# Performance work log

Hardware: AMD Instinct MI355X
Metric: run time of the kernel (lower is better)

The kernel has to match this reference:

```python
import jax, jax.numpy as jnp
import numpy as np

N, P, D = 8, 4096, 3


def _chamfer_one_direction(x, y, x_lengths, y_lengths):
    # x: (N,P1,D), y: (N,P2,D); squared-L2 k=1 NN of each x point in y (norm=2 in knn_points)
    P1 = x.shape[1]
    P2 = y.shape[1]
    x2 = jnp.sum(x * x, axis=-1)  # (N,P1)
    y2 = jnp.sum(y * y, axis=-1)  # (N,P2)
    d2 = x2[:, :, None] + y2[:, None, :] - 2.0 * jnp.einsum('npd,nqd->npq', x, y)  # (N,P1,P2)
    # mask padded y points out of the NN search
    y_mask = jnp.arange(P2)[None, :] >= y_lengths[:, None]  # (N,P2) True = padded
    d2 = jnp.where(y_mask[:, None, :], jnp.inf, d2)
    cham = jnp.min(d2, axis=2)  # (N,P1) dist to nearest valid y
    # zero out padded x points
    x_mask = jnp.arange(P1)[None, :] >= x_lengths[:, None]  # (N,P1)
    cham = jnp.where(x_mask, 0.0, cham)
    # point_reduction='mean'
    per_cloud = jnp.sum(cham, axis=1) / jnp.maximum(x_lengths, 1).astype(x.dtype)  # (N,)
    # batch_reduction='mean' (no weights -> divide by N)
    return jnp.sum(per_cloud) / x.shape[0]


def setup_inputs() -> dict:
    key = jax.random.key(0)
    k1, k2, k3, k4 = jax.random.split(key, 4)
    x = jax.random.normal(k1, (N, P, D), dtype=jnp.float32)
    y = jax.random.normal(k2, (N, P, D), dtype=jnp.float32)
    x_lengths = jax.random.randint(k3, (N,), P // 2, P + 1)
    y_lengths = jax.random.randint(k4, (N,), P // 2, P + 1)
    return {"x": x, "y": y, "x_lengths": x_lengths, "y_lengths": y_lengths}


def reference(x, y, x_lengths, y_lengths):
    cham_x = _chamfer_one_direction(x, y, x_lengths, y_lengths)
    cham_y = _chamfer_one_direction(y, x, y_lengths, x_lengths)
    return cham_x + cham_y
```

## Files before the change

kernel.cpp:

```cpp
#include <hip/hip_runtime.h>
#include <hip/hip_bf16.h>
#include <math.h>

constexpr int NB  = 8;
constexpr int PP  = 4096;

constexpr int TPB = 256;
constexpr int XPT = 8;
constexpr int XCH = TPB * XPT;
constexpr int NXC = PP / XCH;
constexpr int NYC = 32;
constexpr int JH  = 2;
constexpr int JCH = 64;
constexpr int NCH = NYC * JH;
constexpr int GRIDA = 2 * NB * NXC * NYC * JH;

constexpr int NSEG = 16;
constexpr int SEGP = PP / NSEG;
constexpr int NPART = 2 * NB * NSEG;

__global__ __launch_bounds__(TPB, 4) void nn_partial(
    const float* __restrict__ x, const float* __restrict__ y,
    const int* __restrict__ xlen, const int* __restrict__ ylen,
    float* __restrict__ ws)
{
    __shared__ float4 sy[JCH];

    const int bid = (int)blockIdx.x;
    const int jh  = bid & (JH - 1);
    const int yc  = (bid >> 1) & (NYC - 1);
    const int xc  = (bid >> 6) & (NXC - 1);
    const int n   = (bid >> 7) & (NB - 1);
    const int dir = bid >> 10;

    const float* __restrict__ xs = dir ? y : x;
    const float* __restrict__ ys = dir ? x : y;
    const int yl = (dir ? xlen : ylen)[n];
    const int ql = (dir ? ylen : xlen)[n];

    const float* __restrict__ yb = ys + (size_t)n * PP * 3;
    if ((int)threadIdx.x < JCH) {
        const int p   = (int)threadIdx.x;
        const int idx = yc + NYC * (jh * JCH + p);
        float y0 = yb[idx * 3 + 0];
        float y1 = yb[idx * 3 + 1];
        float y2 = yb[idx * 3 + 2];
        sy[p] = make_float4(-2.f * y0, -2.f * y1, -2.f * y2,
                            fmaf(y0, y0, fmaf(y1, y1, y2 * y2)));
    }

    const int wave  = (int)threadIdx.x >> 6;
    const int lane  = (int)threadIdx.x & 63;
    const int wbase = xc * XCH + wave * (XPT * 64);

    float px0[XPT], px1[XPT], px2[XPT], a[XPT], emin[XPT];
    const float* __restrict__ xb = xs + (size_t)n * PP * 3;
#pragma unroll
    for (int k = 0; k < XPT; ++k) {
        const int xi = wbase + k * 64 + lane;
        px0[k] = xb[xi * 3 + 0];
        px1[k] = xb[xi * 3 + 1];
        px2[k] = xb[xi * 3 + 2];
        a[k]   = fmaf(px0[k], px0[k], fmaf(px1[k], px1[k], px2[k] * px2[k]));
        emin[k] = INFINITY;
    }
    __syncthreads();

    int jslice = (yl - yc + NYC - 1) >> 5;
    int jcnt = jslice - jh * JCH;
    if (jcnt > JCH) jcnt = JCH;

    if (ql > wbase && jcnt > 0) {
        const int j2 = jcnt & ~1;
#pragma unroll 2
        for (int j = 0; j < j2; j += 2) {
            const float4 u = sy[j];
            const float4 v = sy[j + 1];
#pragma unroll
            for (int k = 0; k < XPT; ++k) {
                float e1 = fmaf(px0[k], u.x, fmaf(px1[k], u.y, fmaf(px2[k], u.z, u.w)));
                float e2 = fmaf(px0[k], v.x, fmaf(px1[k], v.y, fmaf(px2[k], v.z, v.w)));
                emin[k] = fminf(emin[k], fminf(e1, e2));
            }
        }
        if (jcnt & 1) {
            const float4 u = sy[jcnt - 1];
#pragma unroll
            for (int k = 0; k < XPT; ++k) {
                float e1 = fmaf(px0[k], u.x, fmaf(px1[k], u.y, fmaf(px2[k], u.z, u.w)));
                emin[k] = fminf(emin[k], e1);
            }
        }
    }

    float* __restrict__ w = ws + ((size_t)(dir * NB + n) * NCH + (yc * JH + jh)) * PP;
#pragma unroll
    for (int k = 0; k < XPT; ++k) {
        w[wbase + k * 64 + lane] = a[k] + emin[k];
    }
}

__global__ __launch_bounds__(256) void reduce_cloud(
    const float* __restrict__ ws,
    const int* __restrict__ xlen, const int* __restrict__ ylen,
    float* __restrict__ partial)
{
    const int b   = blockIdx.x;
    const int seg = b & (NSEG - 1);
    const int c   = b >> 4;
    const int dir = c >> 3;
    const int n   = c & (NB - 1);
    const int xl  = (dir ? ylen : xlen)[n];

    const float* __restrict__ w = ws + (size_t)c * NCH * PP;
    const int i = seg * SEGP + (int)threadIdx.x;

    float m = w[i];
#pragma unroll
    for (int ch = 1; ch < NCH; ++ch) m = fminf(m, w[(size_t)ch * PP + i]);
    float sum = (i < xl) ? m : 0.f;

#pragma unroll
    for (int off = 32; off > 0; off >>= 1) sum += __shfl_xor(sum, off);
    __shared__ float ls[4];
    const int lane = (int)threadIdx.x & 63;
    const int wv   = (int)threadIdx.x >> 6;
    if (lane == 0) ls[wv] = sum;
    __syncthreads();
    if (threadIdx.x == 0) {
        float tot = ls[0] + ls[1] + ls[2] + ls[3];
        int d = xl > 1 ? xl : 1;
        partial[b] = tot / (float)d / (float)NB;
    }
}

__global__ __launch_bounds__(256) void final_sum(
    const float* __restrict__ partial, float* __restrict__ out)
{
    float v = partial[threadIdx.x];
#pragma unroll
    for (int off = 32; off > 0; off >>= 1) v += __shfl_xor(v, off);
    __shared__ float ls[4];
    const int lane = (int)threadIdx.x & 63;
    const int wv   = (int)threadIdx.x >> 6;
    if (lane == 0) ls[wv] = v;
    __syncthreads();
    if (threadIdx.x == 0) out[0] = ls[0] + ls[1] + ls[2] + ls[3];
}

__global__ __launch_bounds__(TPB) void chamfer_atomic(
    const float* __restrict__ x, const float* __restrict__ y,
    const int* __restrict__ xlen, const int* __restrict__ ylen,
    float* __restrict__ out)
{
    __shared__ float4 sy[JCH];

    int bid = blockIdx.x;
    const int xc  = bid & (NXC - 1);
    const int n   = (bid >> 1) & (NB - 1);
    const int dir = bid >> 4;

    const float* __restrict__ xs = dir ? y : x;
    const float* __restrict__ ys = dir ? x : y;
    const int yl = (dir ? xlen : ylen)[n];
    const int xl = (dir ? ylen : xlen)[n];

    float px0[XPT], px1[XPT], px2[XPT], a[XPT], emin[XPT];
    const int wave  = (int)threadIdx.x >> 6;
    const int lane  = (int)threadIdx.x & 63;
    const int wbase = xc * XCH + wave * (XPT * 64);
    const float* __restrict__ xb = xs + (size_t)n * PP * 3;
#pragma unroll
    for (int k = 0; k < XPT; ++k) {
        const int xi = wbase + k * 64 + lane;
        px0[k] = xb[xi * 3 + 0];
        px1[k] = xb[xi * 3 + 1];
        px2[k] = xb[xi * 3 + 2];
        a[k]   = fmaf(px0[k], px0[k], fmaf(px1[k], px1[k], px2[k] * px2[k]));
        emin[k] = INFINITY;
    }

    const float* __restrict__ yb = ys + (size_t)n * PP * 3;
    for (int half = 0; half < NYC * JH; ++half) {
        const int yc = half >> 1, jh = half & 1;
        __syncthreads();
        if ((int)threadIdx.x < JCH) {
            const int p   = (int)threadIdx.x;
            const int idx = yc + NYC * (jh * JCH + p);
            float y0 = yb[idx * 3 + 0];
            float y1 = yb[idx * 3 + 1];
            float y2 = yb[idx * 3 + 2];
            sy[p] = make_float4(-2.f * y0, -2.f * y1, -2.f * y2,
                                fmaf(y0, y0, fmaf(y1, y1, y2 * y2)));
        }
        __syncthreads();
        int jslice = (yl - yc + NYC - 1) >> 5;
        int jcnt = jslice - jh * JCH;
        if (jcnt > JCH) jcnt = JCH;
        for (int j = 0; j < jcnt; ++j) {
            const float4 u = sy[j];
#pragma unroll
            for (int k = 0; k < XPT; ++k) {
                float e = fmaf(px0[k], u.x, fmaf(px1[k], u.y, fmaf(px2[k], u.z, u.w)));
                emin[k] = fminf(emin[k], e);
            }
        }
    }

    float sum = 0.f;
#pragma unroll
    for (int k = 0; k < XPT; ++k) {
        const int xi = wbase + k * 64 + lane;
        if (xi < xl) sum += a[k] + emin[k];
    }
#pragma unroll
    for (int off = 32; off > 0; off >>= 1) sum += __shfl_xor(sum, off);
    __shared__ float ls[4];
    if (lane == 0) ls[wave] = sum;
    __syncthreads();
    if (threadIdx.x == 0) {
        float tot = ls[0] + ls[1] + ls[2] + ls[3];
        int d = xl > 1 ? xl : 1;
        atomicAdd(out, tot / (float)d / (float)NB);
    }
}

extern "C" void kernel_launch(void* const* d_in, const int* in_sizes, int n_in,
                              void* d_out, int out_size, void* d_ws, size_t ws_size,
                              hipStream_t stream) {
    const float* x  = (const float*)d_in[0];
    const float* y  = (const float*)d_in[1];
    const int* xl   = (const int*)d_in[2];
    const int* yl   = (const int*)d_in[3];
    float* out      = (float*)d_out;

    const size_t ws_floats = (size_t)2 * NB * NCH * PP;
    const size_t ws_need   = (ws_floats + NPART) * sizeof(float);

    if (ws_size >= ws_need) {
        float* ws      = (float*)d_ws;
        float* partial = ws + ws_floats;
        nn_partial<<<GRIDA, TPB, 0, stream>>>(x, y, xl, yl, ws);
        reduce_cloud<<<NPART, 256, 0, stream>>>(ws, xl, yl, partial);
        final_sum<<<1, 256, 0, stream>>>(partial, out);
    } else {
        hipMemsetAsync(d_out, 0, sizeof(float), stream);
        const int gridF = 2 * NB * NXC;
        chamfer_atomic<<<gridF, TPB, 0, stream>>>(x, y, xl, yl, out);
    }
}
```

Measured before the change: 33.26 us.

## Replace per-chunk partial-min workspace with atomicMin into compact ordered-key table

Instead of each block writing its partial nearest-neighbour minima to a large per-y-chunk workspace that a second kernel min-reduces, blocks now atomicMin an order-preserving uint encoding of the distance into one entry per query point. The table is initialised with a memset, and a single-block kernel decodes, masks and averages all clouds, replacing the two reduction kernels. Each block now covers 128 y points with 4 x points per thread. This removes the multi-megabyte workspace write and read-back, but adds global atomics and a memset, and makes the final reduction serial on one workgroup.

```diff
diff --git a/kernel.cpp b/kernel.cpp
--- a/kernel.cpp
+++ b/kernel.cpp
@@ -4,32 +4,35 @@
 
 constexpr int NB  = 8;
 constexpr int PP  = 4096;
+constexpr int NC  = 2 * NB;
 
 constexpr int TPB = 256;
-constexpr int XPT = 8;
+constexpr int XPT = 4;
 constexpr int XCH = TPB * XPT;
 constexpr int NXC = PP / XCH;
 constexpr int NYC = 32;
-constexpr int JH  = 2;
-constexpr int JCH = 64;
-constexpr int NCH = NYC * JH;
-constexpr int GRIDA = 2 * NB * NXC * NYC * JH;
-
-constexpr int NSEG = 16;
-constexpr int SEGP = PP / NSEG;
-constexpr int NPART = 2 * NB * NSEG;
+constexpr int YCH = PP / NYC;
+constexpr int GRIDA = 2 * NB * NXC * NYC;
+
+__device__ inline unsigned int fkey(float f) {
+    unsigned int b = __float_as_uint(f);
+    return (b & 0x80000000u) ? ~b : (b | 0x80000000u);
+}
+__device__ inline float fdecode(unsigned int k) {
+    unsigned int b = (k & 0x80000000u) ? (k & 0x7FFFFFFFu) : ~k;
+    return __uint_as_float(b);
+}
 
 __global__ __launch_bounds__(TPB, 4) void nn_partial(
     const float* __restrict__ x, const float* __restrict__ y,
     const int* __restrict__ xlen, const int* __restrict__ ylen,
-    float* __restrict__ ws)
+    unsigned int* __restrict__ tab)
 {
-    __shared__ float4 sy[JCH];
+    __shared__ float4 sy[YCH];
 
     const int bid = (int)blockIdx.x;
-    const int jh  = bid & (JH - 1);
-    const int yc  = (bid >> 1) & (NYC - 1);
-    const int xc  = (bid >> 6) & (NXC - 1);
+    const int yc  = bid & (NYC - 1);
+    const int xc  = (bid >> 5) & (NXC - 1);
     const int n   = (bid >> 7) & (NB - 1);
     const int dir = bid >> 10;
 
@@ -39,9 +42,9 @@
     const int ql = (dir ? ylen : xlen)[n];
 
     const float* __restrict__ yb = ys + (size_t)n * PP * 3;
-    if ((int)threadIdx.x < JCH) {
+    if ((int)threadIdx.x < YCH) {
         const int p   = (int)threadIdx.x;
-        const int idx = yc + NYC * (jh * JCH + p);
+        const int idx = yc + NYC * p;
         float y0 = yb[idx * 3 + 0];
         float y1 = yb[idx * 3 + 1];
         float y2 = yb[idx * 3 + 2];
@@ -66,12 +69,11 @@
     }
     __syncthreads();
 
-    int jslice = (yl - yc + NYC - 1) >> 5;
-    int jcnt = jslice - jh * JCH;
-    if (jcnt > JCH) jcnt = JCH;
-
-    if (ql > wbase && jcnt > 0) {
-        const int j2 = jcnt & ~1;
+    int jend = (yl - yc + NYC - 1) >> 5;
+    if (jend > YCH) jend = YCH;
+
+    if (ql > wbase) {
+        const int j2 = jend & ~1;
 #pragma unroll 2
         for (int j = 0; j < j2; j += 2) {
             const float4 u = sy[j];
@@ -83,69 +85,74 @@
                 emin[k] = fminf(emin[k], fminf(e1, e2));
             }
         }
-        if (jcnt & 1) {
-            const float4 u = sy[jcnt - 1];
+        if (jend & 1) {
+            const float4 u = sy[jend - 1];
 #pragma unroll
             for (int k = 0; k < XPT; ++k) {
                 float e1 = fmaf(px0[k], u.x, fmaf(px1[k], u.y, fmaf(px2[k], u.z, u.w)));
                 emin[k] = fminf(emin[k], e1);
             }
         }
-    }
-
-    float* __restrict__ w = ws + ((size_t)(dir * NB + n) * NCH + (yc * JH + jh)) * PP;
-#pragma unroll
-    for (int k = 0; k < XPT; ++k) {
-        w[wbase + k * 64 + lane] = a[k] + emin[k];
-    }
-}
-
-__global__ __launch_bounds__(256) void reduce_cloud(
-    const float* __restrict__ ws,
+        unsigned int* __restrict__ w = tab + (size_t)(dir * NB + n) * PP;
+#pragma unroll
+        for (int k = 0; k < XPT; ++k) {
+            atomicMin(&w[wbase + k * 64 + lane], fkey(a[k] + emin[k]));
+        }
+    }
+}
+
+__global__ __launch_bounds__(256) void reduce_all(
+    const unsigned int* __restrict__ tab,
     const int* __restrict__ xlen, const int* __restrict__ ylen,
-    float* __restrict__ partial)
+    float* __restrict__ out)
 {
-    const int b   = blockIdx.x;
-    const int seg = b & (NSEG - 1);
-    const int c   = b >> 4;
-    const int dir = c >> 3;
-    const int n   = c & (NB - 1);
-    const int xl  = (dir ? ylen : xlen)[n];
-
-    const float* __restrict__ w = ws + (size_t)c * NCH * PP;
-    const int i = seg * SEGP + (int)threadIdx.x;
-
-    float m = w[i];
-#pragma unroll
-    for (int ch = 1; ch < NCH; ++ch) m = fminf(m, w[(size_t)ch * PP + i]);
-    float sum = (i < xl) ? m : 0.f;
-
-#pragma unroll
-    for (int off = 32; off > 0; off >>= 1) sum += __shfl_xor(sum, off);
-    __shared__ float ls[4];
-    const int lane = (int)threadIdx.x & 63;
-    const int wv   = (int)threadIdx.x >> 6;
-    if (lane == 0) ls[wv] = sum;
+    const int t    = (int)threadIdx.x;
+    const int lane = t & 63;
+    const int wv   = t >> 6;
+
+    float acc[NC];
+#pragma unroll
+    for (int c = 0; c < NC; ++c) acc[c] = 0.f;
+
+#pragma unroll 1
+    for (int c = 0; c < NC; ++c) {
+        const int dir = c >> 3;
+        const int n   = c & (NB - 1);
+        const int xl  = (dir ? ylen : xlen)[n];
+        const unsigned int* __restrict__ w = tab + (size_t)c * PP;
+        unsigned int kv[PP / 256];
+#pragma unroll
+        for (int r = 0; r < PP / 256; ++r) kv[r] = w[r * 256 + t];
+        float s = 0.f;
+#pragma unroll
+        for (int r = 0; r < PP / 256; ++r) {
+            const int i = r * 256 + t;
+            s += (i < xl) ? fdecode(kv[r]) : 0.f;
+        }
+        acc[c] = s;
+    }
+
+    __shared__ float ls[NC][4];
+#pragma unroll
+    for (int c = 0; c < NC; ++c) {
+        float s = acc[c];
+#pragma unroll
+        for (int off = 32; off > 0; off >>= 1) s += __shfl_xor(s, off);
+        if (lane == 0) ls[c][wv] = s;
+    }
     __syncthreads();
-    if (threadIdx.x == 0) {
-        float tot = ls[0] + ls[1] + ls[2] + ls[3];
-        int d = xl > 1 ? xl : 1;
-        partial[b] = tot / (float)d / (float)NB;
-    }
-}
-
-__global__ __launch_bounds__(256) void final_sum(
-    const float* __restrict__ partial, float* __restrict__ out)
-{
-    float v = partial[threadIdx.x];
-#pragma unroll
-    for (int off = 32; off > 0; off >>= 1) v += __shfl_xor(v, off);
-    __shared__ float ls[4];
-    const int lane = (int)threadIdx.x & 63;
-    const int wv   = (int)threadIdx.x >> 6;
-    if (lane == 0) ls[wv] = v;
-    __syncthreads();
-    if (threadIdx.x == 0) out[0] = ls[0] + ls[1] + ls[2] + ls[3];
+    if (t == 0) {
+        float tot = 0.f;
+        for (int c = 0; c < NC; ++c) {
+            const int dir = c >> 3;
+            const int n   = c & (NB - 1);
+            const int xl  = (dir ? ylen : xlen)[n];
+            float s = ls[c][0] + ls[c][1] + ls[c][2] + ls[c][3];
+            int d = xl > 1 ? xl : 1;
+            tot += s / (float)d;
+        }
+        out[0] = tot / (float)NB;
+    }
 }
 
 __global__ __launch_bounds__(TPB) void chamfer_atomic(
@@ -153,12 +160,12 @@
     const int* __restrict__ xlen, const int* __restrict__ ylen,
     float* __restrict__ out)
 {
-    __shared__ float4 sy[JCH];
+    __shared__ float4 sy[YCH];
 
     int bid = blockIdx.x;
     const int xc  = bid & (NXC - 1);
-    const int n   = (bid >> 1) & (NB - 1);
-    const int dir = bid >> 4;
+    const int n   = (bid >> 2) & (NB - 1);
+    const int dir = bid >> 5;
 
     const float* __restrict__ xs = dir ? y : x;
     const float* __restrict__ ys = dir ? x : y;
@@ -181,12 +188,11 @@
     }
 
     const float* __restrict__ yb = ys + (size_t)n * PP * 3;
-    for (int half = 0; half < NYC * JH; ++half) {
-        const int yc = half >> 1, jh = half & 1;
+    for (int yc = 0; yc < NYC; ++yc) {
         __syncthreads();
-        if ((int)threadIdx.x < JCH) {
+        if ((int)threadIdx.x < YCH) {
             const int p   = (int)threadIdx.x;
-            const int idx = yc + NYC * (jh * JCH + p);
+            const int idx = yc + NYC * p;
             float y0 = yb[idx * 3 + 0];
             float y1 = yb[idx * 3 + 1];
             float y2 = yb[idx * 3 + 2];
@@ -194,10 +200,9 @@
                                 fmaf(y0, y0, fmaf(y1, y1, y2 * y2)));
         }
         __syncthreads();
-        int jslice = (yl - yc + NYC - 1) >> 5;
-        int jcnt = jslice - jh * JCH;
-        if (jcnt > JCH) jcnt = JCH;
-        for (int j = 0; j < jcnt; ++j) {
+        int jend = (yl - yc + NYC - 1) >> 5;
+        if (jend > YCH) jend = YCH;
+        for (int j = 0; j < jend; ++j) {
             const float4 u = sy[j];
 #pragma unroll
             for (int k = 0; k < XPT; ++k) {
@@ -234,15 +239,13 @@
     const int* yl   = (const int*)d_in[3];
     float* out      = (float*)d_out;
 
-    const size_t ws_floats = (size_t)2 * NB * NCH * PP;
-    const size_t ws_need   = (ws_floats + NPART) * sizeof(float);
-
-    if (ws_size >= ws_need) {
-        float* ws      = (float*)d_ws;
-        float* partial = ws + ws_floats;
-        nn_partial<<<GRIDA, TPB, 0, stream>>>(x, y, xl, yl, ws);
-        reduce_cloud<<<NPART, 256, 0, stream>>>(ws, xl, yl, partial);
-        final_sum<<<1, 256, 0, stream>>>(partial, out);
+    const size_t tab_bytes = (size_t)NC * PP * sizeof(unsigned int);
+
+    if (ws_size >= tab_bytes) {
+        unsigned int* tab = (unsigned int*)d_ws;
+        hipMemsetAsync(tab, 0xFF, tab_bytes, stream);
+        nn_partial<<<GRIDA, TPB, 0, stream>>>(x, y, xl, yl, tab);
+        reduce_all<<<1, 256, 0, stream>>>(tab, xl, yl, out);
     } else {
         hipMemsetAsync(d_out, 0, sizeof(float), stream);
         const int gridF = 2 * NB * NXC;
```

New measurement: 38.68 us. +16.3%, slower.

## Merge y half-chunks into one block and pad invalid y with infinity

Applied to the files above, without the earlier changes.

Each block now handles a full 128-point strided y slice instead of two 64-point halves. This halves the grid and the workspace, and the reduce kernel reads 32 partial minima per point instead of 64. Padded y points are written to shared memory with w=INFINITY, so the inner loop runs a fixed trip count with no per-slice length bookkeeping and no odd-tail path. The cost is fewer blocks in flight and wasted compute on padded y entries, up to about half of them for short clouds.

```diff
diff --git a/kernel.cpp b/kernel.cpp
--- a/kernel.cpp
+++ b/kernel.cpp
@@ -10,10 +10,8 @@
 constexpr int XCH = TPB * XPT;
 constexpr int NXC = PP / XCH;
 constexpr int NYC = 32;
-constexpr int JH  = 2;
-constexpr int JCH = 64;
-constexpr int NCH = NYC * JH;
-constexpr int GRIDA = 2 * NB * NXC * NYC * JH;
+constexpr int YCH = PP / NYC;
+constexpr int GRIDA = 2 * NB * NXC * NYC;
 
 constexpr int NSEG = 16;
 constexpr int SEGP = PP / NSEG;
@@ -24,14 +22,13 @@
     const int* __restrict__ xlen, const int* __restrict__ ylen,
     float* __restrict__ ws)
 {
-    __shared__ float4 sy[JCH];
+    __shared__ float4 sy[YCH];
 
     const int bid = (int)blockIdx.x;
-    const int jh  = bid & (JH - 1);
-    const int yc  = (bid >> 1) & (NYC - 1);
-    const int xc  = (bid >> 6) & (NXC - 1);
-    const int n   = (bid >> 7) & (NB - 1);
-    const int dir = bid >> 10;
+    const int yc  = bid & (NYC - 1);
+    const int xc  = (bid >> 5) & (NXC - 1);
+    const int n   = (bid >> 6) & (NB - 1);
+    const int dir = bid >> 9;
 
     const float* __restrict__ xs = dir ? y : x;
     const float* __restrict__ ys = dir ? x : y;
@@ -39,14 +36,18 @@
     const int ql = (dir ? ylen : xlen)[n];
 
     const float* __restrict__ yb = ys + (size_t)n * PP * 3;
-    if ((int)threadIdx.x < JCH) {
+    if ((int)threadIdx.x < YCH) {
         const int p   = (int)threadIdx.x;
-        const int idx = yc + NYC * (jh * JCH + p);
+        const int idx = yc + NYC * p;
         float y0 = yb[idx * 3 + 0];
         float y1 = yb[idx * 3 + 1];
         float y2 = yb[idx * 3 + 2];
-        sy[p] = make_float4(-2.f * y0, -2.f * y1, -2.f * y2,
-                            fmaf(y0, y0, fmaf(y1, y1, y2 * y2)));
+        if (idx < yl) {
+            sy[p] = make_float4(-2.f * y0, -2.f * y1, -2.f * y2,
+                                fmaf(y0, y0, fmaf(y1, y1, y2 * y2)));
+        } else {
+            sy[p] = make_float4(-0.f, -0.f, -0.f, INFINITY);
+        }
     }
 
     const int wave  = (int)threadIdx.x >> 6;
@@ -66,14 +67,9 @@
     }
     __syncthreads();
 
-    int jslice = (yl - yc + NYC - 1) >> 5;
-    int jcnt = jslice - jh * JCH;
-    if (jcnt > JCH) jcnt = JCH;
-
-    if (ql > wbase && jcnt > 0) {
-        const int j2 = jcnt & ~1;
+    if (ql > wbase) {
 #pragma unroll 2
-        for (int j = 0; j < j2; j += 2) {
+        for (int j = 0; j < YCH; j += 2) {
             const float4 u = sy[j];
             const float4 v = sy[j + 1];
 #pragma unroll
@@ -83,17 +79,9 @@
                 emin[k] = fminf(emin[k], fminf(e1, e2));
             }
         }
-        if (jcnt & 1) {
-            const float4 u = sy[jcnt - 1];
-#pragma unroll
-            for (int k = 0; k < XPT; ++k) {
-                float e1 = fmaf(px0[k], u.x, fmaf(px1[k], u.y, fmaf(px2[k], u.z, u.w)));
-                emin[k] = fminf(emin[k], e1);
-            }
-        }
-    }
-
-    float* __restrict__ w = ws + ((size_t)(dir * NB + n) * NCH + (yc * JH + jh)) * PP;
+    }
+
+    float* __restrict__ w = ws + ((size_t)(dir * NB + n) * NYC + yc) * PP;
 #pragma unroll
     for (int k = 0; k < XPT; ++k) {
         w[wbase + k * 64 + lane] = a[k] + emin[k];
@@ -112,12 +100,12 @@
     const int n   = c & (NB - 1);
     const int xl  = (dir ? ylen : xlen)[n];
 
-    const float* __restrict__ w = ws + (size_t)c * NCH * PP;
+    const float* __restrict__ w = ws + (size_t)c * NYC * PP;
     const int i = seg * SEGP + (int)threadIdx.x;
 
     float m = w[i];
 #pragma unroll
-    for (int ch = 1; ch < NCH; ++ch) m = fminf(m, w[(size_t)ch * PP + i]);
+    for (int ch = 1; ch < NYC; ++ch) m = fminf(m, w[(size_t)ch * PP + i]);
     float sum = (i < xl) ? m : 0.f;
 
 #pragma unroll
@@ -153,7 +141,7 @@
     const int* __restrict__ xlen, const int* __restrict__ ylen,
     float* __restrict__ out)
 {
-    __shared__ float4 sy[JCH];
+    __shared__ float4 sy[YCH];
 
     int bid = blockIdx.x;
     const int xc  = bid & (NXC - 1);
@@ -181,23 +169,23 @@
     }
 
     const float* __restrict__ yb = ys + (size_t)n * PP * 3;
-    for (int half = 0; half < NYC * JH; ++half) {
-        const int yc = half >> 1, jh = half & 1;
+    for (int yc = 0; yc < NYC; ++yc) {
         __syncthreads();
-        if ((int)threadIdx.x < JCH) {
+        if ((int)threadIdx.x < YCH) {
             const int p   = (int)threadIdx.x;
-            const int idx = yc + NYC * (jh * JCH + p);
+            const int idx = yc + NYC * p;
             float y0 = yb[idx * 3 + 0];
             float y1 = yb[idx * 3 + 1];
             float y2 = yb[idx * 3 + 2];
-            sy[p] = make_float4(-2.f * y0, -2.f * y1, -2.f * y2,
-                                fmaf(y0, y0, fmaf(y1, y1, y2 * y2)));
+            if (idx < yl) {
+                sy[p] = make_float4(-2.f * y0, -2.f * y1, -2.f * y2,
+                                    fmaf(y0, y0, fmaf(y1, y1, y2 * y2)));
+            } else {
+                sy[p] = make_float4(-0.f, -0.f, -0.f, INFINITY);
+            }
         }
         __syncthreads();
-        int jslice = (yl - yc + NYC - 1) >> 5;
-        int jcnt = jslice - jh * JCH;
-        if (jcnt > JCH) jcnt = JCH;
-        for (int j = 0; j < jcnt; ++j) {
+        for (int j = 0; j < YCH; ++j) {
             const float4 u = sy[j];
 #pragma unroll
             for (int k = 0; k < XPT; ++k) {
@@ -234,7 +222,7 @@
     const int* yl   = (const int*)d_in[3];
     float* out      = (float*)d_out;
 
-    const size_t ws_floats = (size_t)2 * NB * NCH * PP;
+    const size_t ws_floats = (size_t)2 * NB * NYC * PP;
     const size_t ws_need   = (ws_floats + NPART) * sizeof(float);
 
     if (ws_size >= ws_need) {
```

Measured after the change: 35.15 us. +5.7%, slower.
